# Kernel tuning notes

Hardware: AMD Instinct MI355X
Metric: run time of the kernel (lower is better)

## Reference

```python
import jax, jax.numpy as jnp
import numpy as np

N_NODES = 100000
N_EDGES = 1600000
C_IN = 128
C_OUT = 128
BN_EPS = 1e-5
LEAKY_SLOPE = 0.01


def setup_inputs() -> dict:
    key = jax.random.key(0)
    k1, k2, k3 = jax.random.split(key, 3)
    x = jax.random.normal(k1, (N_NODES, C_IN), dtype=jnp.float32)
    edge_index = jax.random.randint(k2, (2, N_EDGES), 0, N_NODES, dtype=jnp.int64)
    # GCNConv linear weight (glorot-ish scale) and bias
    W = jax.random.normal(k3, (C_IN, C_OUT), dtype=jnp.float32) * (1.0 / np.sqrt(C_IN))
    bias = jnp.zeros((C_OUT,), dtype=jnp.float32)
    # BatchNorm affine params
    gamma = jnp.ones((C_OUT,), dtype=jnp.float32)
    beta = jnp.zeros((C_OUT,), dtype=jnp.float32)
    return {"x": x, "edge_index": edge_index, "W": W, "bias": bias,
            "gamma": gamma, "beta": beta}


def reference(x, edge_index, W, bias, gamma, beta):
    N = x.shape[0]
    # --- GCNConv (add self loops, symmetric degree normalization) ---
    loop = jnp.arange(N, dtype=edge_index.dtype)
    src = jnp.concatenate([edge_index[0], loop])  # message sources (x_j)
    dst = jnp.concatenate([edge_index[1], loop])  # aggregation targets
    ones = jnp.ones(src.shape[0], dtype=x.dtype)
    deg = jax.ops.segment_sum(ones, dst, num_segments=N)
    dinv_sqrt = jnp.where(deg > 0, jax.lax.rsqrt(deg), 0.0).astype(x.dtype)
    norm = dinv_sqrt[src] * dinv_sqrt[dst]  # [E+N]

    h = x @ W                                # [N, C_out], transform first
    msg = h[src] * norm[:, None]             # gather + edge weighting
    out = jax.ops.segment_sum(msg, dst, num_segments=N) + bias  # scatter-add

    # --- LeakyReLU ---
    out = jax.nn.leaky_relu(out, negative_slope=LEAKY_SLOPE)

    # --- BatchNorm over nodes (training-mode batch stats, biased var) ---
    mean = out.mean(axis=0)
    var = out.var(axis=0)
    out = (out - mean) * jax.lax.rsqrt(var + BN_EPS) * gamma + beta
    return out
```

## Files before the change

kernel.cpp:

```cpp
#include <hip/hip_runtime.h>

#define N_NODES 100000
#define N_EDGES 1600000
#define C 128
#define LEAKY 0.01f
#define BN_EPS 1e-5f
#define NB1 391
#define NB_C 391
#define PB 391
#define PBLK 4096
#define STASH 8192

typedef __attribute__((ext_vector_type(8))) short short8;
typedef __attribute__((ext_vector_type(4))) float f32x4;

__device__ __forceinline__ unsigned short f2bf(float f) {
    unsigned int u = __builtin_bit_cast(unsigned int, f);
    u += 0x7FFFu + ((u >> 16) & 1u);
    return (unsigned short)(u >> 16);
}
__device__ __forceinline__ float bf2f(unsigned short b) {
    unsigned int u = ((unsigned int)b) << 16;
    return __builtin_bit_cast(float, u);
}

__global__ __launch_bounds__(256) void k_init(float* __restrict__ sums,
                                              float* __restrict__ sumsq,
                                              const float* __restrict__ W,
                                              unsigned short* __restrict__ wt) {
    int i = blockIdx.x * 256 + threadIdx.x;
    if (i < C) { sums[i] = 0.0f; sumsq[i] = 0.0f; }
    if (i < C * C) wt[i] = f2bf(W[(i & 127) * C + (i >> 7)]);
}

__global__ __launch_bounds__(256) void k_coarse(const int* __restrict__ dst,
                                                int* __restrict__ blk_cnt) {
    __shared__ int lh[NB_C];
    int tid = threadIdx.x, blk = blockIdx.x;
    for (int i = tid; i < NB_C; i += 256) lh[i] = 0;
    __syncthreads();
    #pragma unroll
    for (int it = 0; it < PBLK / 256; ++it) {
        int e = blk * PBLK + it * 256 + tid;
        if (e < N_EDGES) atomicAdd(&lh[dst[e] >> 8], 1);
    }
    __syncthreads();
    for (int i = tid; i < NB_C; i += 256) blk_cnt[i * PB + blk] = lh[i];
}

__global__ __launch_bounds__(512) void k_offsets(const int* __restrict__ blk_cnt,
                                                 int* __restrict__ offset,
                                                 int* __restrict__ total) {
    __shared__ int tmp[512];
    int t = threadIdx.x, k = blockIdx.x;
    int v = (t < PB) ? blk_cnt[k * PB + t] : 0;
    tmp[t] = v;
    __syncthreads();
    for (int off = 1; off < 512; off <<= 1) {
        int u = (t >= off) ? tmp[t - off] : 0;
        __syncthreads();
        tmp[t] += u;
        __syncthreads();
    }
    if (t < PB) offset[k * PB + t] = tmp[t] - v;
    if (t == 511) total[k] = tmp[511];
}

__global__ __launch_bounds__(512) void k_cbase(const int* __restrict__ total,
                                               int* __restrict__ cbase,
                                               int* __restrict__ offs) {
    __shared__ int tmp[512];
    int t = threadIdx.x;
    int v = (t < NB_C) ? total[t] : 0;
    tmp[t] = v;
    __syncthreads();
    for (int off = 1; off < 512; off <<= 1) {
        int u = (t >= off) ? tmp[t - off] : 0;
        __syncthreads();
        tmp[t] += u;
        __syncthreads();
    }
    if (t < NB_C) cbase[t] = tmp[t] - v;
    if (t == 0) { cbase[NB_C] = N_EDGES; offs[N_NODES] = N_EDGES; }
}

__global__ __launch_bounds__(256) void k_partition(const int* __restrict__ src,
                                                   const int* __restrict__ dst,
                                                   const int* __restrict__ cbase,
                                                   const int* __restrict__ offset,
                                                   unsigned int* __restrict__ pairs) {
    __shared__ int lh[NB_C];
    __shared__ int lbase[NB_C];
    int tid = threadIdx.x, blk = blockIdx.x;
    for (int i = tid; i < NB_C; i += 256) {
        lh[i] = 0;
        lbase[i] = cbase[i] + offset[i * PB + blk];
    }
    __syncthreads();
    #pragma unroll
    for (int it = 0; it < PBLK / 256; ++it) {
        int e = blk * PBLK + it * 256 + tid;
        if (e < N_EDGES) {
            int d = dst[e];
            int b = d >> 8;
            int r = atomicAdd(&lh[b], 1);
            pairs[lbase[b] + r] = (unsigned int)src[e] | ((unsigned int)(d & 255) << 17);
        }
    }
}

__global__ __launch_bounds__(256) void k_fine(const unsigned int* __restrict__ pairs,
                                              const int* __restrict__ cbase,
                                              float* __restrict__ dinv,
                                              int* __restrict__ offs,
                                              int* __restrict__ srt) {
    __shared__ int hist[256];
    __shared__ int loff[256];
    __shared__ int cnt2[256];
    __shared__ unsigned int stash[STASH];
    int tid = threadIdx.x, blk = blockIdx.x;
    int nbase = blk * 256;
    int nn = (nbase + 256 <= N_NODES) ? 256 : (N_NODES - nbase);
    int ebeg = cbase[blk];
    int ne = cbase[blk + 1] - ebeg;

    hist[tid] = 0; cnt2[tid] = 0;
    __syncthreads();
    for (int k = tid; k < ne; k += 256) {
        unsigned int pk = pairs[ebeg + k];
        if (k < STASH) stash[k] = pk;
        atomicAdd(&hist[pk >> 17], 1);
    }
    __syncthreads();
    if (tid < nn) dinv[nbase + tid] = rsqrtf((float)(hist[tid] + 1));
    loff[tid] = hist[tid];
    __syncthreads();
    for (int off = 1; off < 256; off <<= 1) {
        int u = (tid >= off) ? loff[tid - off] : 0;
        __syncthreads();
        loff[tid] += u;
        __syncthreads();
    }
    loff[tid] -= hist[tid];
    if (tid < nn) offs[nbase + tid] = ebeg + loff[tid];
    __syncthreads();
    for (int k = tid; k < ne; k += 256) {
        unsigned int pk = (k < STASH) ? stash[k] : pairs[ebeg + k];
        int dl = pk >> 17;
        int r = atomicAdd(&cnt2[dl], 1);
        srt[ebeg + loff[dl] + r] = (int)(pk & 0x1FFFFu);
    }
}

__global__ __launch_bounds__(256) void k_gemm(const float* __restrict__ x,
                                              const unsigned short* __restrict__ wt,
                                              const float* __restrict__ dinv,
                                              unsigned short* __restrict__ hs) {
    int tile = blockIdx.x * 4 + (threadIdx.x >> 6);
    if (tile >= N_NODES / 16) return;
    int lane = threadIdx.x & 63;
    int row0 = tile * 16;

    int ar = lane & 15;
    int kg = (lane >> 4) * 8;

    short8 a[4];
    #pragma unroll
    for (int kk = 0; kk < 4; ++kk) {
        const float* p = &x[(size_t)(row0 + ar) * C + kk * 32 + kg];
        float4 p0 = *(const float4*)p;
        float4 p1 = *(const float4*)(p + 4);
        short8 av;
        av[0] = (short)f2bf(p0.x); av[1] = (short)f2bf(p0.y);
        av[2] = (short)f2bf(p0.z); av[3] = (short)f2bf(p0.w);
        av[4] = (short)f2bf(p1.x); av[5] = (short)f2bf(p1.y);
        av[6] = (short)f2bf(p1.z); av[7] = (short)f2bf(p1.w);
        a[kk] = av;
    }

    int rb = (lane >> 4) * 4;
    float dv[4];
    #pragma unroll
    for (int r = 0; r < 4; ++r) dv[r] = dinv[row0 + rb + r];

    #pragma unroll
    for (int ct = 0; ct < 8; ++ct) {
        f32x4 acc = {0.f, 0.f, 0.f, 0.f};
        #pragma unroll
        for (int kk = 0; kk < 4; ++kk) {
            short8 b = *(const short8*)&wt[(size_t)(ct * 16 + ar) * C + kk * 32 + kg];
            acc = __builtin_amdgcn_mfma_f32_16x16x32_bf16(a[kk], b, acc, 0, 0, 0);
        }
        int col = ct * 16 + ar;
        #pragma unroll
        for (int r = 0; r < 4; ++r)
            hs[(size_t)(row0 + rb + r) * C + col] = f2bf(acc[r] * dv[r]);
    }
}

__global__ __launch_bounds__(256) void k_aggregate(const ushort4* __restrict__ h4,
                                                   const int* __restrict__ srt,
                                                   const int* __restrict__ offs,
                                                   const float* __restrict__ dinv,
                                                   const float* __restrict__ bias,
                                                   float* __restrict__ out) {
    int node = blockIdx.x * 8 + (threadIdx.x >> 5);
    int lane = threadIdx.x & 31;

    float dn = dinv[node];
    int beg = offs[node];
    int end = offs[node + 1];

    ushort4 ms = h4[(size_t)node * 32 + lane];
    float ax = bf2f(ms.x), ay = bf2f(ms.y), az = bf2f(ms.z), aw = bf2f(ms.w);

    for (int k = beg; k < end; k += 8) {
        int   idx[8];
        float msk[8];
        #pragma unroll
        for (int i = 0; i < 8; ++i) {
            int ki = k + i;
            msk[i] = (ki < end) ? 1.0f : 0.0f;
            idx[i] = srt[(ki < end) ? ki : end - 1];
        }
        ushort4 m[8];
        #pragma unroll
        for (int i = 0; i < 8; ++i) m[i] = h4[(size_t)idx[i] * 32 + lane];
        #pragma unroll
        for (int i = 0; i < 8; ++i) {
            ax += msk[i] * bf2f(m[i].x);
            ay += msk[i] * bf2f(m[i].y);
            az += msk[i] * bf2f(m[i].z);
            aw += msk[i] * bf2f(m[i].w);
        }
    }

    float4 b = ((const float4*)bias)[lane];
    float4 v;
    v.x = dn * ax + b.x;
    v.y = dn * ay + b.y;
    v.z = dn * az + b.z;
    v.w = dn * aw + b.w;
    v.x = v.x > 0.f ? v.x : LEAKY * v.x;
    v.y = v.y > 0.f ? v.y : LEAKY * v.y;
    v.z = v.z > 0.f ? v.z : LEAKY * v.z;
    v.w = v.w > 0.f ? v.w : LEAKY * v.w;
    ((float4*)out)[(size_t)node * 32 + lane] = v;
}

__global__ __launch_bounds__(256) void k_stats(const float* __restrict__ out,
                                               float* __restrict__ sums,
                                               float* __restrict__ sumsq) {
    int c = threadIdx.x & 127;
    int half = threadIdx.x >> 7;
    int base = blockIdx.x * 256;
    float s = 0.0f, q = 0.0f;
    for (int r = half; r < 256; r += 2) {
        int n = base + r;
        if (n >= N_NODES) break;
        float v = out[(size_t)n * C + c];
        s += v; q += v * v;
    }
    __shared__ float ls[256], lq[256];
    ls[threadIdx.x] = s; lq[threadIdx.x] = q;
    __syncthreads();
    if (threadIdx.x < 128) {
        atomicAdd(&sums[c],  ls[threadIdx.x] + ls[threadIdx.x + 128]);
        atomicAdd(&sumsq[c], lq[threadIdx.x] + lq[threadIdx.x + 128]);
    }
}

__global__ void k_params(const float* __restrict__ sums, const float* __restrict__ sumsq,
                         const float* __restrict__ gamma, const float* __restrict__ beta,
                         float* __restrict__ scale, float* __restrict__ shift) {
    int c = threadIdx.x;
    float inv_n = 1.0f / (float)N_NODES;
    float mean = sums[c] * inv_n;
    float var = sumsq[c] * inv_n - mean * mean;
    float sc = gamma[c] * rsqrtf(var + BN_EPS);
    scale[c] = sc;
    shift[c] = beta[c] - mean * sc;
}

__global__ __launch_bounds__(256) void k_apply(float* __restrict__ out,
                                               const float* __restrict__ scale,
                                               const float* __restrict__ shift) {
    int i = blockIdx.x * 256 + threadIdx.x;
    int c4 = i & 31;
    float4 v = ((float4*)out)[i];
    float4 sc = ((const float4*)scale)[c4];
    float4 sh = ((const float4*)shift)[c4];
    v.x = v.x * sc.x + sh.x;
    v.y = v.y * sc.y + sh.y;
    v.z = v.z * sc.z + sh.z;
    v.w = v.w * sc.w + sh.w;
    ((float4*)out)[i] = v;
}

extern "C" void kernel_launch(void* const* d_in, const int* in_sizes, int n_in,
                              void* d_out, int out_size, void* d_ws, size_t ws_size,
                              hipStream_t stream) {
    const float* x     = (const float*)d_in[0];
    const int*   edge  = (const int*)d_in[1];
    const float* W     = (const float*)d_in[2];
    const float* bias  = (const float*)d_in[3];
    const float* gamma = (const float*)d_in[4];
    const float* beta  = (const float*)d_in[5];
    float* out = (float*)d_out;
    char* ws = (char*)d_ws;

    unsigned short* hs    = (unsigned short*)ws;  ws += (size_t)N_NODES * C * 2;
    unsigned short* wt    = (unsigned short*)ws;  ws += (size_t)C * C * 2;
    unsigned int*   pairs = (unsigned int*)ws;    ws += (size_t)N_EDGES * 4;
    int*   srt     = (int*)ws;                    ws += (size_t)N_EDGES * 4;
    int*   blk_cnt = (int*)ws;                    ws += (size_t)NB_C * PB * 4;
    int*   offset  = (int*)ws;                    ws += (size_t)NB_C * PB * 4;
    int*   total   = (int*)ws;                    ws += 512 * 4;
    int*   cbase   = (int*)ws;                    ws += 512 * 4;
    int*   offs    = (int*)ws;                    ws += (size_t)(N_NODES + 1) * 4;
    float* dinv    = (float*)ws;                  ws += (size_t)N_NODES * 4;
    float* sums    = (float*)ws;                  ws += C * 4;
    float* sumsq   = (float*)ws;                  ws += C * 4;
    float* scale   = (float*)ws;                  ws += C * 4;
    float* shift   = (float*)ws;

    const int* src = edge;
    const int* dst = edge + N_EDGES;

    k_init     <<<C * C / 256,           256, 0, stream>>>(sums, sumsq, W, wt);
    k_coarse   <<<PB,                    256, 0, stream>>>(dst, blk_cnt);
    k_offsets  <<<NB_C,                  512, 0, stream>>>(blk_cnt, offset, total);
    k_cbase    <<<1,                     512, 0, stream>>>(total, cbase, offs);
    k_partition<<<PB,                    256, 0, stream>>>(src, dst, cbase, offset, pairs);
    k_fine     <<<NB_C,                  256, 0, stream>>>(pairs, cbase, dinv, offs, srt);
    k_gemm     <<<(N_NODES / 16 + 3) / 4, 256, 0, stream>>>(x, wt, dinv, hs);
    k_aggregate<<<N_NODES / 8,           256, 0, stream>>>((const ushort4*)hs, srt, offs, dinv, bias, out);
    k_stats    <<<NB1,                   256, 0, stream>>>(out, sums, sumsq);
    k_params   <<<1, 128,                     0, stream>>>(sums, sumsq, gamma, beta, scale, shift);
    k_apply    <<<N_NODES * C / 4 / 256, 256, 0, stream>>>(out, scale, shift);
}
```

Before: 217.3 us.

## Aggregate before transform, fuse BN stats into GEMM epilogue

Reorders the GCN computation to aggregate dinv-scaled bf16 inputs first and apply the weight GEMM afterwards, using linearity. The x-to-bf16 scaling is folded into the fine sort kernel, and the GEMM epilogue now adds bias, applies LeakyReLU and accumulates per-block BatchNorm partial sums, which removes the separate stats pass over the output. The aggregate loop drops masked tail handling in favour of a full-chunk loop plus a scalar remainder, uses nontemporal index loads, and writes bf16 aggregates. The cost is an extra bf16 intermediate buffer and an added rounding of the aggregate to bf16 before the GEMM.

```diff
diff --git a/kernel.cpp b/kernel.cpp
--- a/kernel.cpp
+++ b/kernel.cpp
@@ -5,11 +5,11 @@
 #define C 128
 #define LEAKY 0.01f
 #define BN_EPS 1e-5f
-#define NB1 391
 #define NB_C 391
 #define PB 391
 #define PBLK 4096
 #define STASH 8192
+#define NBG 1563
 
 typedef __attribute__((ext_vector_type(8))) short short8;
 typedef __attribute__((ext_vector_type(4))) float f32x4;
@@ -24,13 +24,10 @@
     return __builtin_bit_cast(float, u);
 }
 
-__global__ __launch_bounds__(256) void k_init(float* __restrict__ sums,
-                                              float* __restrict__ sumsq,
-                                              const float* __restrict__ W,
+__global__ __launch_bounds__(256) void k_init(const float* __restrict__ W,
                                               unsigned short* __restrict__ wt) {
     int i = blockIdx.x * 256 + threadIdx.x;
-    if (i < C) { sums[i] = 0.0f; sumsq[i] = 0.0f; }
-    if (i < C * C) wt[i] = f2bf(W[(i & 127) * C + (i >> 7)]);
+    wt[i] = f2bf(W[(i & 127) * C + (i >> 7)]);
 }
 
 __global__ __launch_bounds__(256) void k_coarse(const int* __restrict__ dst,
@@ -111,9 +108,11 @@
 
 __global__ __launch_bounds__(256) void k_fine(const unsigned int* __restrict__ pairs,
                                               const int* __restrict__ cbase,
+                                              const float* __restrict__ x,
                                               float* __restrict__ dinv,
                                               int* __restrict__ offs,
-                                              int* __restrict__ srt) {
+                                              int* __restrict__ srt,
+                                              unsigned short* __restrict__ xb) {
     __shared__ int hist[256];
     __shared__ int loff[256];
     __shared__ int cnt2[256];
@@ -150,60 +149,23 @@
         int r = atomicAdd(&cnt2[dl], 1);
         srt[ebeg + loff[dl] + r] = (int)(pk & 0x1FFFFu);
     }
-}
-
-__global__ __launch_bounds__(256) void k_gemm(const float* __restrict__ x,
-                                              const unsigned short* __restrict__ wt,
-                                              const float* __restrict__ dinv,
-                                              unsigned short* __restrict__ hs) {
-    int tile = blockIdx.x * 4 + (threadIdx.x >> 6);
-    if (tile >= N_NODES / 16) return;
-    int lane = threadIdx.x & 63;
-    int row0 = tile * 16;
-
-    int ar = lane & 15;
-    int kg = (lane >> 4) * 8;
-
-    short8 a[4];
-    #pragma unroll
-    for (int kk = 0; kk < 4; ++kk) {
-        const float* p = &x[(size_t)(row0 + ar) * C + kk * 32 + kg];
-        float4 p0 = *(const float4*)p;
-        float4 p1 = *(const float4*)(p + 4);
-        short8 av;
-        av[0] = (short)f2bf(p0.x); av[1] = (short)f2bf(p0.y);
-        av[2] = (short)f2bf(p0.z); av[3] = (short)f2bf(p0.w);
-        av[4] = (short)f2bf(p1.x); av[5] = (short)f2bf(p1.y);
-        av[6] = (short)f2bf(p1.z); av[7] = (short)f2bf(p1.w);
-        a[kk] = av;
-    }
-
-    int rb = (lane >> 4) * 4;
-    float dv[4];
-    #pragma unroll
-    for (int r = 0; r < 4; ++r) dv[r] = dinv[row0 + rb + r];
-
-    #pragma unroll
-    for (int ct = 0; ct < 8; ++ct) {
-        f32x4 acc = {0.f, 0.f, 0.f, 0.f};
-        #pragma unroll
-        for (int kk = 0; kk < 4; ++kk) {
-            short8 b = *(const short8*)&wt[(size_t)(ct * 16 + ar) * C + kk * 32 + kg];
-            acc = __builtin_amdgcn_mfma_f32_16x16x32_bf16(a[kk], b, acc, 0, 0, 0);
-        }
-        int col = ct * 16 + ar;
-        #pragma unroll
-        for (int r = 0; r < 4; ++r)
-            hs[(size_t)(row0 + rb + r) * C + col] = f2bf(acc[r] * dv[r]);
-    }
-}
-
-__global__ __launch_bounds__(256) void k_aggregate(const ushort4* __restrict__ h4,
+    for (int t = tid; t < nn * 32; t += 256) {
+        int r = t >> 5, c4 = t & 31;
+        float dv = rsqrtf((float)(hist[r] + 1));
+        size_t q = ((size_t)(nbase + r) << 5) + c4;
+        float4 xv = ((const float4*)x)[q];
+        ushort4 o;
+        o.x = f2bf(xv.x * dv); o.y = f2bf(xv.y * dv);
+        o.z = f2bf(xv.z * dv); o.w = f2bf(xv.w * dv);
+        ((ushort4*)xb)[q] = o;
+    }
+}
+
+__global__ __launch_bounds__(256) void k_aggregate(const ushort4* __restrict__ xb4,
                                                    const int* __restrict__ srt,
                                                    const int* __restrict__ offs,
                                                    const float* __restrict__ dinv,
-                                                   const float* __restrict__ bias,
-                                                   float* __restrict__ out) {
+                                                   unsigned long long* __restrict__ agg8) {
     int node = blockIdx.x * 8 + (threadIdx.x >> 5);
     int lane = threadIdx.x & 31;
 
@@ -211,75 +173,112 @@
     int beg = offs[node];
     int end = offs[node + 1];
 
-    ushort4 ms = h4[(size_t)node * 32 + lane];
+    ushort4 ms = xb4[(size_t)node * 32 + lane];
     float ax = bf2f(ms.x), ay = bf2f(ms.y), az = bf2f(ms.z), aw = bf2f(ms.w);
 
-    for (int k = beg; k < end; k += 8) {
-        int   idx[8];
-        float msk[8];
+    int k = beg;
+    for (; k + 8 <= end; k += 8) {
+        int idx[8];
+        #pragma unroll
+        for (int i = 0; i < 8; ++i) idx[i] = __builtin_nontemporal_load(&srt[k + i]);
+        ushort4 m[8];
+        #pragma unroll
+        for (int i = 0; i < 8; ++i) m[i] = xb4[(size_t)idx[i] * 32 + lane];
         #pragma unroll
         for (int i = 0; i < 8; ++i) {
-            int ki = k + i;
-            msk[i] = (ki < end) ? 1.0f : 0.0f;
-            idx[i] = srt[(ki < end) ? ki : end - 1];
+            ax += bf2f(m[i].x); ay += bf2f(m[i].y);
+            az += bf2f(m[i].z); aw += bf2f(m[i].w);
         }
-        ushort4 m[8];
-        #pragma unroll
-        for (int i = 0; i < 8; ++i) m[i] = h4[(size_t)idx[i] * 32 + lane];
-        #pragma unroll
-        for (int i = 0; i < 8; ++i) {
-            ax += msk[i] * bf2f(m[i].x);
-            ay += msk[i] * bf2f(m[i].y);
-            az += msk[i] * bf2f(m[i].z);
-            aw += msk[i] * bf2f(m[i].w);
+    }
+    for (; k < end; ++k) {
+        int s = __builtin_nontemporal_load(&srt[k]);
+        ushort4 m = xb4[(size_t)s * 32 + lane];
+        ax += bf2f(m.x); ay += bf2f(m.y); az += bf2f(m.z); aw += bf2f(m.w);
+    }
+
+    ushort4 o;
+    o.x = f2bf(dn * ax); o.y = f2bf(dn * ay);
+    o.z = f2bf(dn * az); o.w = f2bf(dn * aw);
+    unsigned long long packed = __builtin_bit_cast(unsigned long long, o);
+    __builtin_nontemporal_store(packed, &agg8[(size_t)node * 32 + lane]);
+}
+
+__global__ __launch_bounds__(256) void k_gemm(const unsigned short* __restrict__ agg,
+                                              const unsigned short* __restrict__ wt,
+                                              const float* __restrict__ bias,
+                                              float* __restrict__ out,
+                                              float* __restrict__ part) {
+    __shared__ float lsum[C], lsq[C];
+    for (int i = threadIdx.x; i < C; i += 256) { lsum[i] = 0.0f; lsq[i] = 0.0f; }
+    __syncthreads();
+
+    int tile = blockIdx.x * 4 + (threadIdx.x >> 6);
+    int lane = threadIdx.x & 63;
+    if (tile < N_NODES / 16) {
+        int row0 = tile * 16;
+        int ar = lane & 15;
+        int kg = (lane >> 4) * 8;
+
+        short8 a[4];
+        #pragma unroll
+        for (int kk = 0; kk < 4; ++kk)
+            a[kk] = *(const short8*)&agg[(size_t)(row0 + ar) * C + kk * 32 + kg];
+
+        int rb = (lane >> 4) * 4;
+        #pragma unroll
+        for (int ct = 0; ct < 8; ++ct) {
+            f32x4 acc = {0.f, 0.f, 0.f, 0.f};
+            #pragma unroll
+            for (int kk = 0; kk < 4; ++kk) {
+                short8 b = *(const short8*)&wt[(size_t)(ct * 16 + ar) * C + kk * 32 + kg];
+                acc = __builtin_amdgcn_mfma_f32_16x16x32_bf16(a[kk], b, acc, 0, 0, 0);
+            }
+            int col = ct * 16 + ar;
+            float bb = bias[col];
+            float s = 0.0f, q = 0.0f;
+            #pragma unroll
+            for (int r = 0; r < 4; ++r) {
+                float v = acc[r] + bb;
+                v = v > 0.0f ? v : LEAKY * v;
+                out[(size_t)(row0 + rb + r) * C + col] = v;
+                s += v; q += v * v;
+            }
+            atomicAdd(&lsum[col], s);
+            atomicAdd(&lsq[col], q);
         }
     }
-
-    float4 b = ((const float4*)bias)[lane];
-    float4 v;
-    v.x = dn * ax + b.x;
-    v.y = dn * ay + b.y;
-    v.z = dn * az + b.z;
-    v.w = dn * aw + b.w;
-    v.x = v.x > 0.f ? v.x : LEAKY * v.x;
-    v.y = v.y > 0.f ? v.y : LEAKY * v.y;
-    v.z = v.z > 0.f ? v.z : LEAKY * v.z;
-    v.w = v.w > 0.f ? v.w : LEAKY * v.w;
-    ((float4*)out)[(size_t)node * 32 + lane] = v;
-}
-
-__global__ __launch_bounds__(256) void k_stats(const float* __restrict__ out,
-                                               float* __restrict__ sums,
-                                               float* __restrict__ sumsq) {
-    int c = threadIdx.x & 127;
-    int half = threadIdx.x >> 7;
-    int base = blockIdx.x * 256;
+    __syncthreads();
+    for (int i = threadIdx.x; i < C; i += 256) {
+        part[(size_t)blockIdx.x * 256 + i]       = lsum[i];
+        part[(size_t)blockIdx.x * 256 + 128 + i] = lsq[i];
+    }
+}
+
+__global__ __launch_bounds__(1024) void k_params(const float* __restrict__ part,
+                                                 const float* __restrict__ gamma,
+                                                 const float* __restrict__ beta,
+                                                 float* __restrict__ scale,
+                                                 float* __restrict__ shift) {
+    __shared__ float rs[1024], rq[1024];
+    int c = threadIdx.x & 127, g = threadIdx.x >> 7;
     float s = 0.0f, q = 0.0f;
-    for (int r = half; r < 256; r += 2) {
-        int n = base + r;
-        if (n >= N_NODES) break;
-        float v = out[(size_t)n * C + c];
-        s += v; q += v * v;
-    }
-    __shared__ float ls[256], lq[256];
-    ls[threadIdx.x] = s; lq[threadIdx.x] = q;
+    for (int b = g; b < NBG; b += 8) {
+        s += part[(size_t)b * 256 + c];
+        q += part[(size_t)b * 256 + 128 + c];
+    }
+    rs[threadIdx.x] = s; rq[threadIdx.x] = q;
     __syncthreads();
     if (threadIdx.x < 128) {
-        atomicAdd(&sums[c],  ls[threadIdx.x] + ls[threadIdx.x + 128]);
-        atomicAdd(&sumsq[c], lq[threadIdx.x] + lq[threadIdx.x + 128]);
-    }
-}
-
-__global__ void k_params(const float* __restrict__ sums, const float* __restrict__ sumsq,
-                         const float* __restrict__ gamma, const float* __restrict__ beta,
-                         float* __restrict__ scale, float* __restrict__ shift) {
-    int c = threadIdx.x;
-    float inv_n = 1.0f / (float)N_NODES;
-    float mean = sums[c] * inv_n;
-    float var = sumsq[c] * inv_n - mean * mean;
-    float sc = gamma[c] * rsqrtf(var + BN_EPS);
-    scale[c] = sc;
-    shift[c] = beta[c] - mean * sc;
+        float S = 0.0f, Q = 0.0f;
+        #pragma unroll
+        for (int g2 = 0; g2 < 8; ++g2) { S += rs[g2 * 128 + c]; Q += rq[g2 * 128 + c]; }
+        float inv_n = 1.0f / (float)N_NODES;
+        float mean = S * inv_n;
+        float var = Q * inv_n - mean * mean;
+        float sc = gamma[c] * rsqrtf(var + BN_EPS);
+        scale[c] = sc;
+        shift[c] = beta[c] - mean * sc;
+    }
 }
 
 __global__ __launch_bounds__(256) void k_apply(float* __restrict__ out,
@@ -309,7 +308,8 @@
     float* out = (float*)d_out;
     char* ws = (char*)d_ws;
 
-    unsigned short* hs    = (unsigned short*)ws;  ws += (size_t)N_NODES * C * 2;
+    unsigned short* xb    = (unsigned short*)ws;  ws += (size_t)N_NODES * C * 2;
+    unsigned short* agg   = (unsigned short*)ws;  ws += (size_t)N_NODES * C * 2;
     unsigned short* wt    = (unsigned short*)ws;  ws += (size_t)C * C * 2;
     unsigned int*   pairs = (unsigned int*)ws;    ws += (size_t)N_EDGES * 4;
     int*   srt     = (int*)ws;                    ws += (size_t)N_EDGES * 4;
@@ -319,23 +319,21 @@
     int*   cbase   = (int*)ws;                    ws += 512 * 4;
     int*   offs    = (int*)ws;                    ws += (size_t)(N_NODES + 1) * 4;
     float* dinv    = (float*)ws;                  ws += (size_t)N_NODES * 4;
-    float* sums    = (float*)ws;                  ws += C * 4;
-    float* sumsq   = (float*)ws;                  ws += C * 4;
+    float* part    = (float*)ws;                  ws += (size_t)NBG * 256 * 4;
     float* scale   = (float*)ws;                  ws += C * 4;
     float* shift   = (float*)ws;
 
     const int* src = edge;
     const int* dst = edge + N_EDGES;
 
-    k_init     <<<C * C / 256,           256, 0, stream>>>(sums, sumsq, W, wt);
+    k_init     <<<C * C / 256,           256, 0, stream>>>(W, wt);
     k_coarse   <<<PB,                    256, 0, stream>>>(dst, blk_cnt);
     k_offsets  <<<NB_C,                  512, 0, stream>>>(blk_cnt, offset, total);
     k_cbase    <<<1,                     512, 0, stream>>>(total, cbase, offs);
     k_partition<<<PB,                    256, 0, stream>>>(src, dst, cbase, offset, pairs);
-    k_fine     <<<NB_C,                  256, 0, stream>>>(pairs, cbase, dinv, offs, srt);
-    k_gemm     <<<(N_NODES / 16 + 3) / 4, 256, 0, stream>>>(x, wt, dinv, hs);
-    k_aggregate<<<N_NODES / 8,           256, 0, stream>>>((const ushort4*)hs, srt, offs, dinv, bias, out);
-    k_stats    <<<NB1,                   256, 0, stream>>>(out, sums, sumsq);
-    k_params   <<<1, 128,                     0, stream>>>(sums, sumsq, gamma, beta, scale, shift);
+    k_fine     <<<NB_C,                  256, 0, stream>>>(pairs, cbase, x, dinv, offs, srt, xb);
+    k_aggregate<<<N_NODES / 8,           256, 0, stream>>>((const ushort4*)xb, srt, offs, dinv, (unsigned long long*)agg);
+    k_gemm     <<<NBG,                   256, 0, stream>>>(agg, wt, bias, out, part);
+    k_params   <<<1,                    1024, 0, stream>>>(part, gamma, beta, scale, shift);
     k_apply    <<<N_NODES * C / 4 / 256, 256, 0, stream>>>(out, scale, shift);
 }
```

Result: slower. 254.6 us (+17.1%).
